# Performance work log

Hardware: AMD Instinct MI355X
Metric: run time of the kernel (lower is better)

The kernel has to match this reference:

```python
import jax, jax.numpy as jnp
import numpy as np

C_IN = 256
K = 4
C_QK = C_IN // K  # 64


def setup_inputs() -> dict:
    key = jax.random.key(0)
    ks = jax.random.split(key, 9)
    B, C, H, W = 4, C_IN, 64, 64
    s = 0.02
    return {
        "x": jax.random.normal(ks[0], (B, C, H, W), dtype=jnp.float32),
        # 1x1 convs stored as dense [out, in] matrices (kernel_size=1)
        "wq": jax.random.normal(ks[1], (C_QK, C), dtype=jnp.float32) * s,
        "bq": jax.random.normal(ks[2], (C_QK,), dtype=jnp.float32) * s,
        "wk": jax.random.normal(ks[3], (C_QK, C), dtype=jnp.float32) * s,
        "bk": jax.random.normal(ks[4], (C_QK,), dtype=jnp.float32) * s,
        "wv": jax.random.normal(ks[5], (C, C), dtype=jnp.float32) * s,
        "bv": jax.random.normal(ks[6], (C,), dtype=jnp.float32) * s,
        "wg": jax.random.normal(ks[7], (C, C), dtype=jnp.float32) * s,
        "bg": jax.random.normal(ks[8], (C,), dtype=jnp.float32) * s,
    }


def reference(x, wq, bq, wk, bk, wv, bv, wg, bg):
    B, C, H, W = x.shape
    N = H * W
    xf = x.reshape(B, C, N)  # [B, C, N]
    # 1x1 conv == per-pixel linear over channels
    q = jnp.einsum("oc,bcn->bon", wq, xf) + bq[None, :, None]  # [B, Cqk, N]
    k = jnp.einsum("oc,bcn->bon", wk, xf) + bk[None, :, None]  # [B, Cqk, N]
    v = jnp.einsum("oc,bcn->bon", wv, xf) + bv[None, :, None]  # [B, C, N]
    # energy[b, n, m] = <q[:, n], k[:, m]>  (n = query pos, m = key pos)
    energy = jnp.einsum("bon,bom->bnm", q, k)  # [B, N, N]
    energy = jax.nn.elu(energy) / N
    # out[b, c, m] = sum_n v[b, c, n] * energy[b, n, m]
    out = jnp.einsum("bcn,bnm->bcm", v, energy).reshape(B, C, H, W)
    out = jnp.einsum("oc,bchw->bohw", wg, out) + bg[None, :, None, None]
    return out
```

## Files before the change

### kernel.cpp

```cpp
#include <hip/hip_runtime.h>

#define B_ 4
#define C_ 256
#define CQK 64
#define N_ 4096
#define SEG 2
#define SEGN (N_ / SEG)
#define NB 128
#define ITERS (SEGN / NB)
#define TS 512

typedef _Float16 f16;
typedef __attribute__((ext_vector_type(8))) _Float16 f16x8;
typedef __attribute__((ext_vector_type(4))) _Float16 f16x4;
typedef __attribute__((ext_vector_type(4))) float f32x4;
typedef __attribute__((ext_vector_type(4))) float float4v;

#define TILE_OFF(l15, quad) ((l15) * 32 + (quad) * 8)

__global__ __launch_bounds__(256) void prep_w(
    const float* __restrict__ wq, const float* __restrict__ wk,
    const float* __restrict__ wv, const float* __restrict__ wg,
    f16* __restrict__ WQt, f16* __restrict__ WKt, f16* __restrict__ WVt,
    f16* __restrict__ WGt) {
  int chunk = blockIdx.x * 256 + threadIdx.x;
  if (chunk >= 20480) return;
  const float* src;
  f16* dst;
  int lo;
  if (chunk < 2048) { src = wq; dst = WQt; lo = chunk * 8; }
  else if (chunk < 4096) { src = wk; dst = WKt; lo = (chunk - 2048) * 8; }
  else if (chunk < 12288) { src = wv; dst = WVt; lo = (chunk - 4096) * 8; }
  else { src = wg; dst = WGt; lo = (chunk - 12288) * 8; }
  int o = lo >> 8, k = lo & 255;
  f16x8 v;
#pragma unroll
  for (int j = 0; j < 8; j++) v[j] = (f16)src[lo + j];
  *(f16x8*)(dst + ((size_t)(o >> 4) * 8 + (k >> 5)) * TS + (o & 15) * 32 + (k & 31)) = v;
}

__global__ __launch_bounds__(512) void proj(
    const float* __restrict__ x, const f16* __restrict__ WQt,
    const f16* __restrict__ WKt, const f16* __restrict__ WVt,
    const float* __restrict__ bq, const float* __restrict__ bk,
    const float* __restrict__ bv, f16* __restrict__ QTt, f16* __restrict__ KTt,
    f16* __restrict__ Vt) {
  __shared__ float xs[64][65];
  __shared__ f16 xt[4 * 8 * TS];
  int n0 = blockIdx.x * 64;
  int b = blockIdx.y;
  int tid = threadIdx.x, lane = tid & 63, w = tid >> 6;
  int l15 = lane & 15, quad = lane >> 4;
  const float* xb = x + (size_t)b * C_ * N_;

  for (int cc = 0; cc < 4; cc++) {
#pragma unroll
    for (int i = 0; i < 8; i++)
      xs[lane][w * 8 + i] = xb[(size_t)(cc * 64 + w * 8 + i) * N_ + n0 + lane];
    __syncthreads();
    {
      int nt = w >> 1;
      f16x8 v;
#pragma unroll
      for (int j = 0; j < 8; j++)
        v[j] = (f16)xs[nt * 16 + l15][32 * (w & 1) + quad * 8 + j];
      *(f16x8*)(xt + (nt * 8 + cc * 2 + (w & 1)) * TS + l15 * 32 + quad * 8) = v;
    }
    __syncthreads();
  }

  f32x4 acc[3][4];
#pragma unroll
  for (int j = 0; j < 3; j++)
#pragma unroll
    for (int nt = 0; nt < 4; nt++) acc[j][nt] = (f32x4){0.f, 0.f, 0.f, 0.f};

#pragma unroll
  for (int kt = 0; kt < 8; kt++) {
    f16x8 xf[4];
#pragma unroll
    for (int nt = 0; nt < 4; nt++)
      xf[nt] = *(const f16x8*)(xt + (nt * 8 + kt) * TS + TILE_OFF(l15, quad));
#pragma unroll
    for (int j = 0; j < 3; j++) {
      int g = w * 3 + j;
      const f16* Wt;
      int ot;
      bool isV = g < 16;
      if (isV) { Wt = WVt; ot = g; }
      else if (g < 20) { Wt = WQt; ot = g - 16; }
      else { Wt = WKt; ot = g - 20; }
      f16x8 wf = *(const f16x8*)(Wt + ((size_t)ot * 8 + kt) * TS + TILE_OFF(l15, quad));
#pragma unroll
      for (int nt = 0; nt < 4; nt++)
        acc[j][nt] = isV
            ? __builtin_amdgcn_mfma_f32_16x16x32_f16(xf[nt], wf, acc[j][nt], 0, 0, 0)
            : __builtin_amdgcn_mfma_f32_16x16x32_f16(wf, xf[nt], acc[j][nt], 0, 0, 0);
    }
  }

  f16* vbout = Vt + (size_t)b * C_ * N_;
#pragma unroll
  for (int j = 0; j < 3; j++) {
    int g = w * 3 + j;
    if (g < 16) {
      float bvv = bv[16 * g + l15];
#pragma unroll
      for (int nt = 0; nt < 4; nt++) {
        f16x4 vals;
#pragma unroll
        for (int r = 0; r < 4; r++) vals[r] = (f16)(acc[j][nt][r] + bvv);
        *(f16x4*)(vbout + ((size_t)g * 128 + (n0 >> 5) + (nt >> 1)) * TS +
                  l15 * 32 + 16 * (nt & 1) + 4 * quad) = vals;
      }
    } else {
      int oq = (g < 20) ? (g - 16) : (g - 20);
      const float* bias = (g < 20) ? bq : bk;
      f16* ob = ((g < 20) ? QTt : KTt) + (size_t)b * N_ * CQK;
#pragma unroll
      for (int nt = 0; nt < 4; nt++) {
        f16x4 vals;
#pragma unroll
        for (int r = 0; r < 4; r++)
          vals[r] = (f16)(acc[j][nt][r] + bias[16 * oq + 4 * quad + r]);
        *(f16x4*)(ob + (((size_t)(n0 >> 4) + nt) * 2 + (oq >> 1)) * TS + l15 * 32 +
                  16 * (oq & 1) + 4 * quad) = vals;
      }
    }
  }
}

__global__ __launch_bounds__(256, 2) void attn(const f16* __restrict__ qt,
                                               const f16* __restrict__ kt,
                                               const f16* __restrict__ v,
                                               const f16* __restrict__ WGt,
                                               f16* __restrict__ part) {
  __shared__ __align__(16) f16 sPt[2][64][128];
  int sb = blockIdx.x;
  int seg = sb >> 2;
  int b = sb & 3;
  int m0 = blockIdx.y * 64;
  int tid = threadIdx.x, lane = tid & 63, w = tid >> 6;
  int l15 = lane & 15, quad = lane >> 4;
  const f16* qtb = qt + (size_t)b * N_ * CQK;
  const f16* ktb = kt + (size_t)b * N_ * CQK;
  const f16* vb = v + (size_t)b * C_ * N_;

  f32x4 oacc[4][4];
#pragma unroll
  for (int ct = 0; ct < 4; ct++)
#pragma unroll
    for (int mt = 0; mt < 4; mt++) oacc[ct][mt] = (f32x4){0.f, 0.f, 0.f, 0.f};

  f16x8 kf[4][2];
#pragma unroll
  for (int mt = 0; mt < 4; mt++)
#pragma unroll
    for (int ks = 0; ks < 2; ks++)
      kf[mt][ks] = *(const f16x8*)(ktb + ((size_t)((m0 >> 4) + mt) * 2 + ks) * TS +
                                   TILE_OFF(l15, quad));

  f16x8 qf[2][2];
#pragma unroll
  for (int nt = 0; nt < 2; nt++)
#pragma unroll
    for (int ks = 0; ks < 2; ks++)
      qf[nt][ks] = *(const f16x8*)(qtb +
                                   ((size_t)(((seg * SEGN) >> 4) + 2 * w + nt) * 2 + ks) * TS +
                                   TILE_OFF(l15, quad));

  {
    char* buf = (char*)sPt[0];
#pragma unroll
    for (int nt = 0; nt < 2; nt++) {
      f32x4 sacc[4];
#pragma unroll
      for (int mt = 0; mt < 4; mt++) sacc[mt] = (f32x4){0.f, 0.f, 0.f, 0.f};
#pragma unroll
      for (int ks = 0; ks < 2; ks++)
#pragma unroll
        for (int mt = 0; mt < 4; mt++)
          sacc[mt] = __builtin_amdgcn_mfma_f32_16x16x32_f16(qf[nt][ks], kf[mt][ks],
                                                            sacc[mt], 0, 0, 0);
#pragma unroll
      for (int mt = 0; mt < 4; mt++) {
        f16x4 p;
#pragma unroll
        for (int r = 0; r < 4; r++) {
          float s = sacc[mt][r];
          p[r] = (f16)(s > 0.0f ? s : (__expf(s) - 1.0f));
        }
        int row = 16 * mt + l15;
        int colb = (64 * w + 32 * nt + 8 * quad) ^ ((row & 7) << 4);
        *(f16x4*)(buf + row * 256 + colb) = p;
      }
    }
  }
  {
    int nq = seg * SEGN + NB;
#pragma unroll
    for (int nt = 0; nt < 2; nt++)
#pragma unroll
      for (int ks = 0; ks < 2; ks++)
        qf[nt][ks] = *(const f16x8*)(qtb +
                                     ((size_t)((nq >> 4) + 2 * w + nt) * 2 + ks) * TS +
                                     TILE_OFF(l15, quad));
  }
  __syncthreads();

  for (int it = 0; it < ITERS; it++) {
    int n0 = seg * SEGN + it * NB;
    char* rbuf = (char*)sPt[it & 1];
    char* wbuf = (char*)sPt[(it + 1) & 1];
    bool hasNext = (it + 1 < ITERS);

    f16x8 vfA[2][4];
#pragma unroll
    for (int ks = 0; ks < 2; ks++)
#pragma unroll
      for (int ct = 0; ct < 4; ct++)
        vfA[ks][ct] = *(const f16x8*)(vb +
                                      ((size_t)(4 * w + ct) * 128 + (n0 >> 5) + ks) * TS +
                                      TILE_OFF(l15, quad));

    f32x4 s0[4], s1[4];
    if (hasNext) {
#pragma unroll
      for (int mt = 0; mt < 4; mt++) s0[mt] = (f32x4){0.f, 0.f, 0.f, 0.f};
#pragma unroll
      for (int ks = 0; ks < 2; ks++)
#pragma unroll
        for (int mt = 0; mt < 4; mt++)
          s0[mt] = __builtin_amdgcn_mfma_f32_16x16x32_f16(qf[0][ks], kf[mt][ks],
                                                          s0[mt], 0, 0, 0);
    }

    f16x8 pa[4];
#pragma unroll
    for (int mt = 0; mt < 4; mt++) {
      int row = 16 * mt + l15;
      pa[mt] = *(const f16x8*)(rbuf + row * 256 + ((quad * 16) ^ ((row & 7) << 4)));
    }
#pragma unroll
    for (int ct = 0; ct < 4; ct++)
#pragma unroll
      for (int mt = 0; mt < 4; mt++)
        oacc[ct][mt] = __builtin_amdgcn_mfma_f32_16x16x32_f16(vfA[0][ct], pa[mt],
                                                              oacc[ct][mt], 0, 0, 0);

    f16x8 vfB[2][4];
#pragma unroll
    for (int ks = 0; ks < 2; ks++)
#pragma unroll
      for (int ct = 0; ct < 4; ct++)
        vfB[ks][ct] = *(const f16x8*)(vb + ((size_t)(4 * w + ct) * 128 + (n0 >> 5) +
                                            2 + ks) * TS +
                                      TILE_OFF(l15, quad));

    if (hasNext) {
#pragma unroll
      for (int mt = 0; mt < 4; mt++) {
        f16x4 p;
#pragma unroll
        for (int r = 0; r < 4; r++) {
          float s = s0[mt][r];
          p[r] = (f16)(s > 0.0f ? s : (__expf(s) - 1.0f));
        }
        int row = 16 * mt + l15;
        int colb = (64 * w + 8 * quad) ^ ((row & 7) << 4);
        *(f16x4*)(wbuf + row * 256 + colb) = p;
      }
    }

#pragma unroll
    for (int mt = 0; mt < 4; mt++) {
      int row = 16 * mt + l15;
      pa[mt] = *(const f16x8*)(rbuf + row * 256 + ((64 + quad * 16) ^ ((row & 7) << 4)));
    }
#pragma unroll
    for (int ct = 0; ct < 4; ct++)
#pragma unroll
      for (int mt = 0; mt < 4; mt++)
        oacc[ct][mt] = __builtin_amdgcn_mfma_f32_16x16x32_f16(vfA[1][ct], pa[mt],
                                                              oacc[ct][mt], 0, 0, 0);

    if (hasNext) {
#pragma unroll
      for (int mt = 0; mt < 4; mt++) s1[mt] = (f32x4){0.f, 0.f, 0.f, 0.f};
#pragma unroll
      for (int ks = 0; ks < 2; ks++)
#pragma unroll
        for (int mt = 0; mt < 4; mt++)
          s1[mt] = __builtin_amdgcn_mfma_f32_16x16x32_f16(qf[1][ks], kf[mt][ks],
                                                          s1[mt], 0, 0, 0);
    }

#pragma unroll
    for (int mt = 0; mt < 4; mt++) {
      int row = 16 * mt + l15;
      pa[mt] = *(const f16x8*)(rbuf + row * 256 + ((128 + quad * 16) ^ ((row & 7) << 4)));
    }
#pragma unroll
    for (int ct = 0; ct < 4; ct++)
#pragma unroll
      for (int mt = 0; mt < 4; mt++)
        oacc[ct][mt] = __builtin_amdgcn_mfma_f32_16x16x32_f16(vfB[0][ct], pa[mt],
                                                              oacc[ct][mt], 0, 0, 0);

    if (hasNext) {
#pragma unroll
      for (int mt = 0; mt < 4; mt++) {
        f16x4 p;
#pragma unroll
        for (int r = 0; r < 4; r++) {
          float s = s1[mt][r];
          p[r] = (f16)(s > 0.0f ? s : (__expf(s) - 1.0f));
        }
        int row = 16 * mt + l15;
        int colb = (64 * w + 32 + 8 * quad) ^ ((row & 7) << 4);
        *(f16x4*)(wbuf + row * 256 + colb) = p;
      }
      if (it + 2 < ITERS) {
        int nq = seg * SEGN + (it + 2) * NB;
#pragma unroll
        for (int nt = 0; nt < 2; nt++)
#pragma unroll
          for (int ks = 0; ks < 2; ks++)
            qf[nt][ks] = *(const f16x8*)(qtb +
                                         ((size_t)((nq >> 4) + 2 * w + nt) * 2 + ks) * TS +
                                         TILE_OFF(l15, quad));
      }
    }

#pragma unroll
    for (int mt = 0; mt < 4; mt++) {
      int row = 16 * mt + l15;
      pa[mt] = *(const f16x8*)(rbuf + row * 256 + ((192 + quad * 16) ^ ((row & 7) << 4)));
    }
#pragma unroll
    for (int ct = 0; ct < 4; ct++)
#pragma unroll
      for (int mt = 0; mt < 4; mt++)
        oacc[ct][mt] = __builtin_amdgcn_mfma_f32_16x16x32_f16(vfB[1][ct], pa[mt],
                                                              oacc[ct][mt], 0, 0, 0);

    __syncthreads();
  }

  f16* obuf = (f16*)sPt;
#pragma unroll
  for (int ct = 0; ct < 4; ct++) {
#pragma unroll
    for (int mt = 0; mt < 4; mt++) {
      f16x4 vals;
#pragma unroll
      for (int r = 0; r < 4; r++)
        vals[r] = (f16)(oacc[ct][mt][r] * (1.0f / (float)N_));
      *(f16x4*)(obuf + (mt * 8 + 2 * w + (ct >> 1)) * TS + l15 * 32 +
                16 * (ct & 1) + 4 * quad) = vals;
    }
  }
  __syncthreads();
  f32x4 accO[4][4];
#pragma unroll
  for (int ot = 0; ot < 4; ot++)
#pragma unroll
    for (int mt = 0; mt < 4; mt++) accO[ot][mt] = (f32x4){0.f, 0.f, 0.f, 0.f};
#pragma unroll
  for (int kt = 0; kt < 8; kt++) {
    f16x8 bO[4];
#pragma unroll
    for (int mt = 0; mt < 4; mt++)
      bO[mt] = *(const f16x8*)(obuf + (mt * 8 + kt) * TS + TILE_OFF(l15, quad));
#pragma unroll
    for (int ot = 0; ot < 4; ot++) {
      f16x8 af = *(const f16x8*)(WGt + ((size_t)(4 * w + ot) * 8 + kt) * TS +
                                 TILE_OFF(l15, quad));
#pragma unroll
      for (int mt = 0; mt < 4; mt++)
        accO[ot][mt] = __builtin_amdgcn_mfma_f32_16x16x32_f16(af, bO[mt], accO[ot][mt], 0, 0, 0);
    }
  }
  f16* pb = part + ((size_t)(seg * B_ + b) * C_) * N_;
#pragma unroll
  for (int ot = 0; ot < 4; ot++) {
#pragma unroll
    for (int mt = 0; mt < 4; mt++) {
      int m = m0 + 16 * mt + l15;
#pragma unroll
      for (int r = 0; r < 4; r++) {
        int o = 64 * w + 16 * ot + 4 * quad + r;
        pb[(size_t)o * N_ + m] = (f16)accO[ot][mt][r];
      }
    }
  }
}

__global__ __launch_bounds__(256) void combine(const f16* __restrict__ part,
                                               const float* __restrict__ bg,
                                               float* __restrict__ out) {
  size_t i = ((size_t)blockIdx.x * 256 + threadIdx.x) * 8;
  f16x8 p0 = *(const f16x8*)(part + i);
  f16x8 p1 = *(const f16x8*)(part + (size_t)B_ * C_ * N_ + i);
  float bgo = bg[(i >> 12) & 255];
  float4v r0, r1;
#pragma unroll
  for (int j = 0; j < 4; j++) r0[j] = (float)p0[j] + (float)p1[j] + bgo;
#pragma unroll
  for (int j = 0; j < 4; j++) r1[j] = (float)p0[4 + j] + (float)p1[4 + j] + bgo;
  *(float4v*)(out + i) = r0;
  *(float4v*)(out + i + 4) = r1;
}

extern "C" void kernel_launch(void* const* d_in, const int* in_sizes, int n_in,
                              void* d_out, int out_size, void* d_ws, size_t ws_size,
                              hipStream_t stream) {
  const float* x = (const float*)d_in[0];
  const float* wq = (const float*)d_in[1];
  const float* bq = (const float*)d_in[2];
  const float* wk = (const float*)d_in[3];
  const float* bk = (const float*)d_in[4];
  const float* wv = (const float*)d_in[5];
  const float* bv = (const float*)d_in[6];
  const float* wg = (const float*)d_in[7];
  const float* bg = (const float*)d_in[8];
  float* out = (float*)d_out;

  char* ws = (char*)d_ws;
  f16* QTt = (f16*)ws; ws += (size_t)B_ * N_ * CQK * sizeof(f16);
  f16* KTt = (f16*)ws; ws += (size_t)B_ * N_ * CQK * sizeof(f16);
  f16* Vt  = (f16*)ws; ws += (size_t)B_ * C_ * N_ * sizeof(f16);
  f16* WQt = (f16*)ws; ws += (size_t)CQK * C_ * sizeof(f16);
  f16* WKt = (f16*)ws; ws += (size_t)CQK * C_ * sizeof(f16);
  f16* WVt = (f16*)ws; ws += (size_t)C_ * C_ * sizeof(f16);
  f16* WGt = (f16*)ws; ws += (size_t)C_ * C_ * sizeof(f16);
  f16* PART = (f16*)ws; ws += (size_t)SEG * B_ * C_ * N_ * sizeof(f16);

  prep_w<<<dim3(80), 256, 0, stream>>>(wq, wk, wv, wg, WQt, WKt, WVt, WGt);
  proj<<<dim3(N_ / 64, B_), 512, 0, stream>>>(x, WQt, WKt, WVt, bq, bk, bv,
                                              QTt, KTt, Vt);
  attn<<<dim3(SEG * B_, N_ / 64), 256, 0, stream>>>(QTt, KTt, Vt, WGt, PART);
  combine<<<dim3(2048), 256, 0, stream>>>(PART, bg, out);
}
```

Before: 157.3 us.

## Drop weight-prep kernel, convert fp32 weights inside proj/attn, retile projection

Removes the separate prep_w launch that converted and re-tiled weights to fp16. proj and the attn epilogue now read row-major fp32 weights directly and convert them to fp16 MFMA fragments in registers. proj is also retiled to 32 pixels per 256-thread block with six output groups per wave, and x is read with float4 vector loads. This saves one kernel launch and an intermediate buffer, at the cost of twice the weight bytes per fragment load, less contiguous weight access, and repeated conversion work in every block.

Result: slower. 173.7 us (+10.4%).

```diff
diff --git a/kernel.cpp b/kernel.cpp
--- a/kernel.cpp
+++ b/kernel.cpp
@@ -18,36 +18,26 @@
 
 #define TILE_OFF(l15, quad) ((l15) * 32 + (quad) * 8)
 
-__global__ __launch_bounds__(256) void prep_w(
-    const float* __restrict__ wq, const float* __restrict__ wk,
-    const float* __restrict__ wv, const float* __restrict__ wg,
-    f16* __restrict__ WQt, f16* __restrict__ WKt, f16* __restrict__ WVt,
-    f16* __restrict__ WGt) {
-  int chunk = blockIdx.x * 256 + threadIdx.x;
-  if (chunk >= 20480) return;
-  const float* src;
-  f16* dst;
-  int lo;
-  if (chunk < 2048) { src = wq; dst = WQt; lo = chunk * 8; }
-  else if (chunk < 4096) { src = wk; dst = WKt; lo = (chunk - 2048) * 8; }
-  else if (chunk < 12288) { src = wv; dst = WVt; lo = (chunk - 4096) * 8; }
-  else { src = wg; dst = WGt; lo = (chunk - 12288) * 8; }
-  int o = lo >> 8, k = lo & 255;
-  f16x8 v;
-#pragma unroll
-  for (int j = 0; j < 8; j++) v[j] = (f16)src[lo + j];
-  *(f16x8*)(dst + ((size_t)(o >> 4) * 8 + (k >> 5)) * TS + (o & 15) * 32 + (k & 31)) = v;
+__device__ __forceinline__ f16x8 load_wfrag(const float* __restrict__ Ws,
+                                            int row, int col) {
+  const float* p = Ws + (size_t)row * C_ + col;
+  float4v a = *(const float4v*)p;
+  float4v b = *(const float4v*)(p + 4);
+  f16x8 r;
+#pragma unroll
+  for (int j = 0; j < 4; j++) { r[j] = (f16)a[j]; r[4 + j] = (f16)b[j]; }
+  return r;
 }
 
-__global__ __launch_bounds__(512) void proj(
-    const float* __restrict__ x, const f16* __restrict__ WQt,
-    const f16* __restrict__ WKt, const f16* __restrict__ WVt,
+__global__ __launch_bounds__(256) void proj(
+    const float* __restrict__ x, const float* __restrict__ wq,
+    const float* __restrict__ wk, const float* __restrict__ wv,
     const float* __restrict__ bq, const float* __restrict__ bk,
     const float* __restrict__ bv, f16* __restrict__ QTt, f16* __restrict__ KTt,
     f16* __restrict__ Vt) {
-  __shared__ float xs[64][65];
-  __shared__ f16 xt[4 * 8 * TS];
-  int n0 = blockIdx.x * 64;
+  __shared__ float xs[32][65];
+  __shared__ f16 xt[2 * 8 * TS];
+  int n0 = blockIdx.x * 32;
   int b = blockIdx.y;
   int tid = threadIdx.x, lane = tid & 63, w = tid >> 6;
   int l15 = lane & 15, quad = lane >> 4;
@@ -55,8 +45,14 @@
 
   for (int cc = 0; cc < 4; cc++) {
 #pragma unroll
-    for (int i = 0; i < 8; i++)
-      xs[lane][w * 8 + i] = xb[(size_t)(cc * 64 + w * 8 + i) * N_ + n0 + lane];
+    for (int k = 0; k < 2; k++) {
+      int p = w * 2 + k;
+      int c_off = p * 8 + (lane >> 3);
+      int n4 = (lane & 7) * 4;
+      float4v f4 = *(const float4v*)(xb + (size_t)(cc * 64 + c_off) * N_ + n0 + n4);
+#pragma unroll
+      for (int j = 0; j < 4; j++) xs[n4 + j][c_off] = f4[j];
+    }
     __syncthreads();
     {
       int nt = w >> 1;
@@ -69,30 +65,30 @@
     __syncthreads();
   }
 
-  f32x4 acc[3][4];
-#pragma unroll
-  for (int j = 0; j < 3; j++)
-#pragma unroll
-    for (int nt = 0; nt < 4; nt++) acc[j][nt] = (f32x4){0.f, 0.f, 0.f, 0.f};
+  f32x4 acc[6][2];
+#pragma unroll
+  for (int j = 0; j < 6; j++)
+#pragma unroll
+    for (int nt = 0; nt < 2; nt++) acc[j][nt] = (f32x4){0.f, 0.f, 0.f, 0.f};
 
 #pragma unroll
   for (int kt = 0; kt < 8; kt++) {
-    f16x8 xf[4];
-#pragma unroll
-    for (int nt = 0; nt < 4; nt++)
+    f16x8 xf[2];
+#pragma unroll
+    for (int nt = 0; nt < 2; nt++)
       xf[nt] = *(const f16x8*)(xt + (nt * 8 + kt) * TS + TILE_OFF(l15, quad));
 #pragma unroll
-    for (int j = 0; j < 3; j++) {
-      int g = w * 3 + j;
-      const f16* Wt;
+    for (int j = 0; j < 6; j++) {
+      int g = w * 6 + j;
+      const float* Ws;
       int ot;
       bool isV = g < 16;
-      if (isV) { Wt = WVt; ot = g; }
-      else if (g < 20) { Wt = WQt; ot = g - 16; }
-      else { Wt = WKt; ot = g - 20; }
-      f16x8 wf = *(const f16x8*)(Wt + ((size_t)ot * 8 + kt) * TS + TILE_OFF(l15, quad));
-#pragma unroll
-      for (int nt = 0; nt < 4; nt++)
+      if (isV) { Ws = wv; ot = g; }
+      else if (g < 20) { Ws = wq; ot = g - 16; }
+      else { Ws = wk; ot = g - 20; }
+      f16x8 wf = load_wfrag(Ws, ot * 16 + l15, kt * 32 + quad * 8);
+#pragma unroll
+      for (int nt = 0; nt < 2; nt++)
         acc[j][nt] = isV
             ? __builtin_amdgcn_mfma_f32_16x16x32_f16(xf[nt], wf, acc[j][nt], 0, 0, 0)
             : __builtin_amdgcn_mfma_f32_16x16x32_f16(wf, xf[nt], acc[j][nt], 0, 0, 0);
@@ -101,24 +97,24 @@
 
   f16* vbout = Vt + (size_t)b * C_ * N_;
 #pragma unroll
-  for (int j = 0; j < 3; j++) {
-    int g = w * 3 + j;
+  for (int j = 0; j < 6; j++) {
+    int g = w * 6 + j;
     if (g < 16) {
       float bvv = bv[16 * g + l15];
 #pragma unroll
-      for (int nt = 0; nt < 4; nt++) {
+      for (int nt = 0; nt < 2; nt++) {
         f16x4 vals;
 #pragma unroll
         for (int r = 0; r < 4; r++) vals[r] = (f16)(acc[j][nt][r] + bvv);
-        *(f16x4*)(vbout + ((size_t)g * 128 + (n0 >> 5) + (nt >> 1)) * TS +
-                  l15 * 32 + 16 * (nt & 1) + 4 * quad) = vals;
+        *(f16x4*)(vbout + ((size_t)g * 128 + (n0 >> 5)) * TS +
+                  l15 * 32 + 16 * nt + 4 * quad) = vals;
       }
     } else {
       int oq = (g < 20) ? (g - 16) : (g - 20);
       const float* bias = (g < 20) ? bq : bk;
       f16* ob = ((g < 20) ? QTt : KTt) + (size_t)b * N_ * CQK;
 #pragma unroll
-      for (int nt = 0; nt < 4; nt++) {
+      for (int nt = 0; nt < 2; nt++) {
         f16x4 vals;
 #pragma unroll
         for (int r = 0; r < 4; r++)
@@ -133,7 +129,7 @@
 __global__ __launch_bounds__(256, 2) void attn(const f16* __restrict__ qt,
                                                const f16* __restrict__ kt,
                                                const f16* __restrict__ v,
-                                               const f16* __restrict__ WGt,
+                                               const float* __restrict__ wg,
                                                f16* __restrict__ part) {
   __shared__ __align__(16) f16 sPt[2][64][128];
   int sb = blockIdx.x;
@@ -374,8 +370,7 @@
       bO[mt] = *(const f16x8*)(obuf + (mt * 8 + kt) * TS + TILE_OFF(l15, quad));
 #pragma unroll
     for (int ot = 0; ot < 4; ot++) {
-      f16x8 af = *(const f16x8*)(WGt + ((size_t)(4 * w + ot) * 8 + kt) * TS +
-                                 TILE_OFF(l15, quad));
+      f16x8 af = load_wfrag(wg, (4 * w + ot) * 16 + l15, kt * 32 + quad * 8);
 #pragma unroll
       for (int mt = 0; mt < 4; mt++)
         accO[ot][mt] = __builtin_amdgcn_mfma_f32_16x16x32_f16(af, bO[mt], accO[ot][mt], 0, 0, 0);
@@ -430,15 +425,10 @@
   f16* QTt = (f16*)ws; ws += (size_t)B_ * N_ * CQK * sizeof(f16);
   f16* KTt = (f16*)ws; ws += (size_t)B_ * N_ * CQK * sizeof(f16);
   f16* Vt  = (f16*)ws; ws += (size_t)B_ * C_ * N_ * sizeof(f16);
-  f16* WQt = (f16*)ws; ws += (size_t)CQK * C_ * sizeof(f16);
-  f16* WKt = (f16*)ws; ws += (size_t)CQK * C_ * sizeof(f16);
-  f16* WVt = (f16*)ws; ws += (size_t)C_ * C_ * sizeof(f16);
-  f16* WGt = (f16*)ws; ws += (size_t)C_ * C_ * sizeof(f16);
   f16* PART = (f16*)ws; ws += (size_t)SEG * B_ * C_ * N_ * sizeof(f16);
 
-  prep_w<<<dim3(80), 256, 0, stream>>>(wq, wk, wv, wg, WQt, WKt, WVt, WGt);
-  proj<<<dim3(N_ / 64, B_), 512, 0, stream>>>(x, WQt, WKt, WVt, bq, bk, bv,
+  proj<<<dim3(N_ / 32, B_), 256, 0, stream>>>(x, wq, wk, wv, bq, bk, bv,
                                               QTt, KTt, Vt);
-  attn<<<dim3(SEG * B_, N_ / 64), 256, 0, stream>>>(QTt, KTt, Vt, WGt, PART);
+  attn<<<dim3(SEG * B_, N_ / 64), 256, 0, stream>>>(QTt, KTt, Vt, wg, PART);
   combine<<<dim3(2048), 256, 0, stream>>>(PART, bg, out);
 }
```
